# Performance work log

Hardware: AMD Instinct MI355X
Metric: run time of the kernel (lower is better)

Reference implementation:

```python
import jax, jax.numpy as jnp
import numpy as np

NUM_USERS = 100000
NUM_ITEMS = 50000
EMB_DIM = 128
NUM_LAYERS = 3
NUM_EDGES = 2000000
BATCH = 8192
REG = 1e-4


def setup_inputs() -> dict:
    key = jax.random.key(0)
    ks = jax.random.split(key, 8)
    N = NUM_USERS + NUM_ITEMS
    user_emb = jax.random.normal(ks[0], (NUM_USERS, EMB_DIM), dtype=jnp.float32) * 0.01
    item_emb = jax.random.normal(ks[1], (NUM_ITEMS, EMB_DIM), dtype=jnp.float32) * 0.01
    edge_row = jax.random.randint(ks[2], (NUM_EDGES,), 0, N, dtype=jnp.int32)
    edge_col = jax.random.randint(ks[3], (NUM_EDGES,), 0, N, dtype=jnp.int32)
    # symmetric-normalized adjacency values are small positives
    edge_val = jax.random.uniform(ks[4], (NUM_EDGES,), dtype=jnp.float32) * 0.1
    user = jax.random.randint(ks[5], (BATCH,), 0, NUM_USERS, dtype=jnp.int32)
    pos = jax.random.randint(ks[6], (BATCH,), 0, NUM_ITEMS, dtype=jnp.int32)
    neg = jax.random.randint(ks[7], (BATCH,), 0, NUM_ITEMS, dtype=jnp.int32)
    return {"user_emb": user_emb, "item_emb": item_emb,
            "edge_row": edge_row, "edge_col": edge_col, "edge_val": edge_val,
            "user": user, "pos": pos, "neg": neg}


def _lightgcn_embedding(user_emb, item_emb, edge_row, edge_col, edge_val):
    N = user_emb.shape[0] + item_emb.shape[0]
    emb = jnp.concatenate([user_emb, item_emb], axis=0)  # [N, D]
    acc = emb
    for _ in range(NUM_LAYERS):
        # SpMM: out[r] += val * emb[c] for each edge (r, c)
        msg = emb[edge_col] * edge_val[:, None]  # [E, D]
        emb = jax.ops.segment_sum(msg, edge_row, num_segments=N)
        acc = acc + emb
    light = acc / jnp.float32(NUM_LAYERS + 1)  # mean over layer outputs
    return light[:NUM_USERS], light[NUM_USERS:]


def reference(user_emb, item_emb, edge_row, edge_col, edge_val, user, pos, neg):
    u_all, i_all = _lightgcn_embedding(user_emb, item_emb, edge_row, edge_col, edge_val)
    u_lat = u_all[user]          # [B, D]
    pos_lat = i_all[pos]
    neg_lat = i_all[neg]
    pos_score = jnp.sum(u_lat * pos_lat, axis=1)
    neg_score = jnp.sum(u_lat * neg_lat, axis=1)
    # L1 regularization on ego (layer-0) embeddings, scalar broadcast onto batch loss
    reg_loss = REG * (jnp.sum(jnp.abs(user_emb[user]))
                      + jnp.sum(jnp.abs(item_emb[pos]))
                      + jnp.sum(jnp.abs(item_emb[neg])))
    batch_loss = jax.nn.softplus(neg_score - pos_score) + reg_loss
    return batch_loss
```

## Files before the change

### kernel.cpp

```cpp
#include <hip/hip_runtime.h>
#include <hip/hip_bf16.h>

#define EMB_D 128
#define BSH 9
#define MAXBUCK 512
#define CHUNKP 2048

typedef float f32x2 __attribute__((ext_vector_type(2)));

__device__ __forceinline__ float bf16_raw_to_f(unsigned short h) {
    return __uint_as_float(((unsigned int)h) << 16);
}
__device__ __forceinline__ float sane(float v) {
    return (v == v && fabsf(v) < 256.0f) ? v : 0.0f;
}
__device__ __forceinline__ float load_f(const void* p, int isf32, size_t idx) {
    return isf32 ? ((const float*)p)[idx]
                 : bf16_raw_to_f(((const unsigned short*)p)[idx]);
}

__device__ __forceinline__ f32x2 cvt2_fp8(unsigned int w) {
    f32x2 r;
    asm("v_cvt_pk_f32_fp8 %0, %1" : "=v"(r) : "v"(w));
    return r;
}
__device__ __forceinline__ unsigned int enc2_fp8(float a, float b) {
    unsigned int r;
    asm("v_cvt_pk_fp8_f32 %0, %1, %2" : "=v"(r) : "v"(a), "v"(b));
    return r & 0xFFFFu;
}
__device__ __forceinline__ unsigned int fp8x4_enc(float a, float b, float c, float d) {
    return enc2_fp8(a, b) | (enc2_fp8(c, d) << 16);
}
__device__ __forceinline__ float fp8_dec_byte(unsigned int b) {
    return cvt2_fp8(b & 0xFFu).x;
}

__global__ void k_detect(const unsigned short* __restrict__ ue,
                         const unsigned short* __restrict__ ie,
                         const unsigned short* __restrict__ ev,
                         int* __restrict__ flags) {
    int a = blockIdx.x;
    const unsigned short* p = (a == 0) ? ue : (a == 1) ? ie : ev;
    int lane = threadIdx.x;
    int cnt = 0;
    #pragma unroll
    for (int k = 0; k < 16; ++k) {
        float v = bf16_raw_to_f(p[k * 64 + lane]);
        if (!(fabsf(v) < 1.0f)) cnt++;
    }
    #pragma unroll
    for (int off = 32; off > 0; off >>= 1)
        cnt += __shfl_down(cnt, off, 64);
    if (lane == 0) flags[a] = (cnt > 64) ? 1 : 0;
}

__global__ __launch_bounds__(256) void k_build_emb8(
        const void* __restrict__ ue, const void* __restrict__ ie,
        const int* __restrict__ flags,
        unsigned char* __restrict__ T, float* __restrict__ S,
        int NU, int N) {
    int gid = blockIdx.x * blockDim.x + threadIdx.x;
    int row = gid >> 5;
    if (row >= N) return;
    int l = gid & 31;
    const void* src; long r; int f;
    if (row < NU) { src = ue; r = row;      f = flags[0]; }
    else          { src = ie; r = row - NU; f = flags[1]; }
    float v0, v1, v2, v3;
    if (f) {
        float4 t = ((const float4*)src)[r * 32 + l];
        v0 = sane(t.x); v1 = sane(t.y); v2 = sane(t.z); v3 = sane(t.w);
    } else {
        ushort4 t = ((const ushort4*)src)[r * 32 + l];
        v0 = sane(bf16_raw_to_f(t.x)); v1 = sane(bf16_raw_to_f(t.y));
        v2 = sane(bf16_raw_to_f(t.z)); v3 = sane(bf16_raw_to_f(t.w));
    }
    float m = fmaxf(fmaxf(fabsf(v0), fabsf(v1)), fmaxf(fabsf(v2), fabsf(v3)));
    #pragma unroll
    for (int off = 1; off < 32; off <<= 1)
        m = fmaxf(m, __shfl_xor(m, off, 64));
    float enc = (m > 0.0f) ? 448.0f / m : 0.0f;
    ((unsigned int*)T)[(size_t)row * 32 + l] =
        fp8x4_enc(v0 * enc, v1 * enc, v2 * enc, v3 * enc);
    if (l == 0) S[row] = (m > 0.0f) ? m * (1.0f / 448.0f) : 0.0f;
}

__global__ void k_reg(const void* __restrict__ ue, const void* __restrict__ ie,
                      const int* __restrict__ flags,
                      const int* __restrict__ user, const int* __restrict__ pos,
                      const int* __restrict__ neg, int NU, int NI,
                      float* __restrict__ regp) {
    __shared__ float sred[2];
    int b = blockIdx.x;
    int d = threadIdx.x;
    int ui = min(max(user[b], 0), NU - 1);
    int pi = min(max(pos[b],  0), NI - 1);
    int ni = min(max(neg[b],  0), NI - 1);
    int f0 = flags[0], f1 = flags[1];
    float u = sane(load_f(ue, f0, (size_t)ui * EMB_D + d));
    float p = sane(load_f(ie, f1, (size_t)pi * EMB_D + d));
    float n = sane(load_f(ie, f1, (size_t)ni * EMB_D + d));
    float s = fabsf(u) + fabsf(p) + fabsf(n);
    #pragma unroll
    for (int off = 32; off > 0; off >>= 1)
        s += __shfl_down(s, off, 64);
    if ((d & 63) == 0) sred[d >> 6] = s;
    __syncthreads();
    if (d == 0) regp[b] = sred[0] + sred[1];
}

__global__ void k_reduce_reg(const float* __restrict__ regp, float* __restrict__ reg, int B) {
    __shared__ float ss[256];
    int t = threadIdx.x;
    float s = 0.0f;
    for (int i = t; i < B; i += 256) s += regp[i];
    ss[t] = s;
    __syncthreads();
    for (int off = 128; off > 0; off >>= 1) {
        if (t < off) ss[t] += ss[t + off];
        __syncthreads();
    }
    if (t == 0) reg[0] = ss[0];
}


__global__ __launch_bounds__(256) void k_part_count(const int* __restrict__ erow,
        int* __restrict__ bcnt, int E, int N, int nbuck, int NB) {
    __shared__ int lh[MAXBUCK];
    int b = blockIdx.x, t = threadIdx.x;
    for (int i = t; i < MAXBUCK; i += 256) lh[i] = 0;
    __syncthreads();
    int beg = b * CHUNKP;
    int cnt = min(CHUNKP, E - beg);
    for (int p = t; p < cnt; p += 256) {
        int r = min(max(erow[beg + p], 0), N - 1);
        atomicAdd(&lh[r >> BSH], 1);
    }
    __syncthreads();
    for (int i = t; i < nbuck; i += 256) bcnt[(long)i * NB + b] = lh[i];
}

__global__ void k_gscan1(const int* __restrict__ a, int* __restrict__ bsums, int L) {
    __shared__ int ss[256];
    int t = threadIdx.x;
    int base = blockIdx.x * 1024 + t * 4;
    int s = 0;
    #pragma unroll
    for (int j = 0; j < 4; ++j) {
        int idx = base + j;
        if (idx < L) s += a[idx];
    }
    ss[t] = s;
    __syncthreads();
    for (int off = 128; off > 0; off >>= 1) {
        if (t < off) ss[t] += ss[t + off];
        __syncthreads();
    }
    if (t == 0) bsums[blockIdx.x] = ss[0];
}

__global__ void k_gscan2(const int* __restrict__ bsums, int* __restrict__ boffs,
                         int nb, int* __restrict__ rowptrN) {
    __shared__ int ss[256];
    int t = threadIdx.x;
    int base = t * 4;
    int c[4];
    int s = 0;
    #pragma unroll
    for (int j = 0; j < 4; ++j) {
        c[j] = (base + j < nb) ? bsums[base + j] : 0;
        s += c[j];
    }
    ss[t] = s;
    __syncthreads();
    for (int off = 1; off < 256; off <<= 1) {
        int v = (t >= off) ? ss[t - off] : 0;
        __syncthreads();
        ss[t] += v;
        __syncthreads();
    }
    int run = ss[t] - s;
    #pragma unroll
    for (int j = 0; j < 4; ++j) {
        if (base + j < nb) boffs[base + j] = run;
        run += c[j];
    }
    if (t == 255) *rowptrN = ss[255];
}

__global__ void k_gscan3(int* __restrict__ a, const int* __restrict__ boffs, int L) {
    __shared__ int ss[256];
    int t = threadIdx.x;
    int base = blockIdx.x * 1024 + t * 4;
    int c[4];
    int s = 0;
    #pragma unroll
    for (int j = 0; j < 4; ++j) {
        int idx = base + j;
        c[j] = (idx < L) ? a[idx] : 0;
        s += c[j];
    }
    ss[t] = s;
    __syncthreads();
    for (int off = 1; off < 256; off <<= 1) {
        int v = (t >= off) ? ss[t - off] : 0;
        __syncthreads();
        ss[t] += v;
        __syncthreads();
    }
    int run = boffs[blockIdx.x] + ss[t] - s;
    #pragma unroll
    for (int j = 0; j < 4; ++j) {
        int idx = base + j;
        if (idx < L) a[idx] = run;
        run += c[j];
    }
}

__global__ __launch_bounds__(256) void k_part_scatter(
        const int* __restrict__ erow, const int* __restrict__ ecol,
        const void* __restrict__ eval, const int* __restrict__ flags,
        const int* __restrict__ boff,
        unsigned int* __restrict__ part_cv, unsigned short* __restrict__ part_r,
        int E, int N, int nbuck, int NB) {
    __shared__ uint2 lrec[CHUNKP];
    __shared__ unsigned short lidx[CHUNKP];
    __shared__ int hist[MAXBUCK];
    __shared__ int bstart[MAXBUCK];
    __shared__ int ss[256];
    int b = blockIdx.x, t = threadIdx.x;
    int beg = b * CHUNKP;
    int cnt = min(CHUNKP, E - beg);
    for (int i = t; i < MAXBUCK; i += 256) hist[i] = 0;
    __syncthreads();
    int f2 = flags[2];
    for (int p = t; p < cnt; p += 256) {
        int e = beg + p;
        int r = min(max(erow[e], 0), N - 1);
        int c = min(max(ecol[e], 0), N - 1);
        float v = sane(load_f(eval, f2, e));
        if (v < 0.0f) v = 0.0f;
        unsigned int u = __float_as_uint(v);
        unsigned int vb = ((u + 0x10000u) >> 17) & 0x3FFFu;
        lrec[p] = make_uint2((unsigned int)r, ((unsigned int)c << 14) | vb);
        atomicAdd(&hist[r >> BSH], 1);
    }
    __syncthreads();
    int c0 = hist[2 * t], c1 = hist[2 * t + 1];
    int s = c0 + c1;
    ss[t] = s;
    __syncthreads();
    for (int off = 1; off < 256; off <<= 1) {
        int v = (t >= off) ? ss[t - off] : 0;
        __syncthreads();
        ss[t] += v;
        __syncthreads();
    }
    int eb = ss[t] - s;
    bstart[2 * t] = eb;
    bstart[2 * t + 1] = eb + c0;
    hist[2 * t] = eb;
    hist[2 * t + 1] = eb + c0;
    __syncthreads();
    for (int p = t; p < cnt; p += 256) {
        int bin = (int)(lrec[p].x >> BSH);
        int pos = atomicAdd(&hist[bin], 1);
        lidx[pos] = (unsigned short)p;
    }
    __syncthreads();
    for (int i = t; i < nbuck; i += 256)
        hist[i] = boff[(long)i * NB + b] - bstart[i];
    __syncthreads();
    for (int p = t; p < cnt; p += 256) {
        uint2 rec = lrec[lidx[p]];
        int bin = (int)(rec.x >> BSH);
        int o = hist[bin] + p;
        part_cv[o] = rec.y;
        part_r[o] = (unsigned short)(rec.x & 511u);
    }
}

__global__ __launch_bounds__(256) void k_build_csr(
        const unsigned int* __restrict__ part_cv,
        const unsigned short* __restrict__ part_r,
        const int* __restrict__ boff,
        int* __restrict__ row_ptr, unsigned int* __restrict__ sedge,
        int E, int N, int NB, int nbuck) {
    __shared__ int rcnt[512];
    __shared__ int rstart[512];
    __shared__ int rcur[512];
    __shared__ int ss[256];
    int bin = blockIdx.x, t = threadIdx.x;
    int base = boff[(long)bin * NB];
    int next = (bin + 1 < nbuck) ? boff[(long)(bin + 1) * NB] : E;
    int cnt = next - base;
    int r0 = bin << BSH;
    int nrows = min(512, N - r0);
    rcnt[2 * t] = 0; rcnt[2 * t + 1] = 0;
    __syncthreads();
    for (int i = t; i < cnt; i += 256)
        atomicAdd(&rcnt[part_r[base + i]], 1);
    __syncthreads();
    int c0 = rcnt[2 * t], c1 = rcnt[2 * t + 1];
    int s = c0 + c1;
    ss[t] = s;
    __syncthreads();
    for (int off = 1; off < 256; off <<= 1) {
        int v = (t >= off) ? ss[t - off] : 0;
        __syncthreads();
        ss[t] += v;
        __syncthreads();
    }
    int eb = ss[t] - s;
    rstart[2 * t] = eb; rstart[2 * t + 1] = eb + c0;
    rcur[2 * t]   = eb; rcur[2 * t + 1]   = eb + c0;
    __syncthreads();
    for (int j = t; j < nrows; j += 256)
        row_ptr[r0 + j] = base + rstart[j];
    for (int i = t; i < cnt; i += 256) {
        int pr = part_r[base + i];
        int pos = atomicAdd(&rcur[pr], 1);
        sedge[base + pos] = part_cv[base + i];
    }
}


__global__ void k_zero_flags(int* __restrict__ f, int words) {
    int i = blockIdx.x * blockDim.x + threadIdx.x;
    if (i < words) f[i] = 0;
}

__global__ void k_mark_batch(const int* __restrict__ user, const int* __restrict__ pos,
                             const int* __restrict__ neg, int NU, int NI, int B,
                             unsigned char* __restrict__ flag3,
                             unsigned char* __restrict__ flag2) {
    int b = blockIdx.x * blockDim.x + threadIdx.x;
    if (b >= B) return;
    int ui = min(max(user[b], 0), NU - 1);
    int pi = NU + min(max(pos[b], 0), NI - 1);
    int ni = NU + min(max(neg[b], 0), NI - 1);
    flag3[ui] = 1; flag3[pi] = 1; flag3[ni] = 1;
    flag2[ui] = 1; flag2[pi] = 1; flag2[ni] = 1;
}

__global__ void k_mark_nbrs(const int* __restrict__ row_ptr,
                            const unsigned int* __restrict__ sedge,
                            const unsigned char* __restrict__ flag3,
                            unsigned char* __restrict__ flag2, int N) {
    int r = blockIdx.x * blockDim.x + threadIdx.x;
    if (r >= N || !flag3[r]) return;
    int beg = row_ptr[r], end = row_ptr[r + 1];
    for (int i = beg; i < end; ++i)
        flag2[sedge[i] >> 14] = 1;
}


__global__ void k_spmm_csr8(const unsigned char* __restrict__ T,
                            const float* __restrict__ S,
                            unsigned char* __restrict__ Td,
                            float* __restrict__ Sd,
                            const int* __restrict__ row_ptr,
                            const unsigned int* __restrict__ sedge, int N,
                            const unsigned char* __restrict__ skipf, int use_skip) {
    int row = blockIdx.x * (blockDim.x >> 6) + (threadIdx.x >> 6);
    if (row >= N) return;
    if (use_skip && skipf[row] == 0) return;
    int lane = threadIdx.x & 63;
    int sub = lane >> 3;
    int sl  = lane & 7;
    int beg = row_ptr[row], end = row_ptr[row + 1];
    float a[16];
    #pragma unroll
    for (int j = 0; j < 16; ++j) a[j] = 0.0f;
    int i = beg + sub;
    for (; i + 8 < end; i += 16) {
        unsigned int se0 = sedge[i];
        unsigned int se1 = sedge[i + 8];
        unsigned int c0 = se0 >> 14, c1 = se1 >> 14;
        uint4 h0 = ((const uint4*)(T + (size_t)c0 * EMB_D))[sl];
        uint4 h1 = ((const uint4*)(T + (size_t)c1 * EMB_D))[sl];
        float vs0 = __uint_as_float((se0 & 0x3FFFu) << 17) * S[c0];
        float vs1 = __uint_as_float((se1 & 0x3FFFu) << 17) * S[c1];
        f32x2 d;
        d = cvt2_fp8(h0.x);       a[0] += vs0 * d.x;  a[1] += vs0 * d.y;
        d = cvt2_fp8(h0.x >> 16); a[2] += vs0 * d.x;  a[3] += vs0 * d.y;
        d = cvt2_fp8(h0.y);       a[4] += vs0 * d.x;  a[5] += vs0 * d.y;
        d = cvt2_fp8(h0.y >> 16); a[6] += vs0 * d.x;  a[7] += vs0 * d.y;
        d = cvt2_fp8(h0.z);       a[8] += vs0 * d.x;  a[9] += vs0 * d.y;
        d = cvt2_fp8(h0.z >> 16); a[10] += vs0 * d.x; a[11] += vs0 * d.y;
        d = cvt2_fp8(h0.w);       a[12] += vs0 * d.x; a[13] += vs0 * d.y;
        d = cvt2_fp8(h0.w >> 16); a[14] += vs0 * d.x; a[15] += vs0 * d.y;
        d = cvt2_fp8(h1.x);       a[0] += vs1 * d.x;  a[1] += vs1 * d.y;
        d = cvt2_fp8(h1.x >> 16); a[2] += vs1 * d.x;  a[3] += vs1 * d.y;
        d = cvt2_fp8(h1.y);       a[4] += vs1 * d.x;  a[5] += vs1 * d.y;
        d = cvt2_fp8(h1.y >> 16); a[6] += vs1 * d.x;  a[7] += vs1 * d.y;
        d = cvt2_fp8(h1.z);       a[8] += vs1 * d.x;  a[9] += vs1 * d.y;
        d = cvt2_fp8(h1.z >> 16); a[10] += vs1 * d.x; a[11] += vs1 * d.y;
        d = cvt2_fp8(h1.w);       a[12] += vs1 * d.x; a[13] += vs1 * d.y;
        d = cvt2_fp8(h1.w >> 16); a[14] += vs1 * d.x; a[15] += vs1 * d.y;
    }
    if (i < end) {
        unsigned int se = sedge[i];
        unsigned int c = se >> 14;
        uint4 h = ((const uint4*)(T + (size_t)c * EMB_D))[sl];
        float vs = __uint_as_float((se & 0x3FFFu) << 17) * S[c];
        f32x2 d;
        d = cvt2_fp8(h.x);       a[0] += vs * d.x;  a[1] += vs * d.y;
        d = cvt2_fp8(h.x >> 16); a[2] += vs * d.x;  a[3] += vs * d.y;
        d = cvt2_fp8(h.y);       a[4] += vs * d.x;  a[5] += vs * d.y;
        d = cvt2_fp8(h.y >> 16); a[6] += vs * d.x;  a[7] += vs * d.y;
        d = cvt2_fp8(h.z);       a[8] += vs * d.x;  a[9] += vs * d.y;
        d = cvt2_fp8(h.z >> 16); a[10] += vs * d.x; a[11] += vs * d.y;
        d = cvt2_fp8(h.w);       a[12] += vs * d.x; a[13] += vs * d.y;
        d = cvt2_fp8(h.w >> 16); a[14] += vs * d.x; a[15] += vs * d.y;
    }
    #pragma unroll
    for (int j = 0; j < 16; ++j) {
        a[j] += __shfl_xor(a[j], 8, 64);
        a[j] += __shfl_xor(a[j], 16, 64);
        a[j] += __shfl_xor(a[j], 32, 64);
    }
    float m = 0.0f;
    #pragma unroll
    for (int j = 0; j < 16; ++j) m = fmaxf(m, fabsf(a[j]));
    m = fmaxf(m, __shfl_xor(m, 1, 64));
    m = fmaxf(m, __shfl_xor(m, 2, 64));
    m = fmaxf(m, __shfl_xor(m, 4, 64));
    if (sub == 0) {
        float enc = (m > 0.0f) ? 448.0f / m : 0.0f;
        uint4 w;
        w.x = fp8x4_enc(a[0] * enc,  a[1] * enc,  a[2] * enc,  a[3] * enc);
        w.y = fp8x4_enc(a[4] * enc,  a[5] * enc,  a[6] * enc,  a[7] * enc);
        w.z = fp8x4_enc(a[8] * enc,  a[9] * enc,  a[10] * enc, a[11] * enc);
        w.w = fp8x4_enc(a[12] * enc, a[13] * enc, a[14] * enc, a[15] * enc);
        ((uint4*)(Td + (size_t)row * EMB_D))[sl] = w;
        if (lane == 0) Sd[row] = (m > 0.0f) ? m * (1.0f / 448.0f) : 0.0f;
    }
}

__global__ void k_gather_final(
        const void* __restrict__ ue, const void* __restrict__ ie,
        const int* __restrict__ flags,
        const int* __restrict__ user, const int* __restrict__ pos,
        const int* __restrict__ neg, int NU, int NI,
        const unsigned char* __restrict__ T1, const float* __restrict__ S1,
        const unsigned char* __restrict__ T2, const float* __restrict__ S2,
        const unsigned char* __restrict__ T3, const float* __restrict__ S3,
        const float* __restrict__ reg, float* __restrict__ out) {
    __shared__ float sps[2], sns[2];
    int b = blockIdx.x;
    int d = threadIdx.x;
    int ui = min(max(user[b], 0), NU - 1);
    int pi = min(max(pos[b],  0), NI - 1);
    int ni = min(max(neg[b],  0), NI - 1);
    size_t ru = (size_t)ui;
    size_t rp = (size_t)NU + pi;
    size_t rn = (size_t)NU + ni;
    int f0 = flags[0], f1 = flags[1];
    float u = sane(load_f(ue, f0, ru * EMB_D + d))
            + fp8_dec_byte(T1[ru * EMB_D + d]) * S1[ru]
            + fp8_dec_byte(T2[ru * EMB_D + d]) * S2[ru]
            + fp8_dec_byte(T3[ru * EMB_D + d]) * S3[ru];
    float p = sane(load_f(ie, f1, (size_t)pi * EMB_D + d))
            + fp8_dec_byte(T1[rp * EMB_D + d]) * S1[rp]
            + fp8_dec_byte(T2[rp * EMB_D + d]) * S2[rp]
            + fp8_dec_byte(T3[rp * EMB_D + d]) * S3[rp];
    float n = sane(load_f(ie, f1, (size_t)ni * EMB_D + d))
            + fp8_dec_byte(T1[rn * EMB_D + d]) * S1[rn]
            + fp8_dec_byte(T2[rn * EMB_D + d]) * S2[rn]
            + fp8_dec_byte(T3[rn * EMB_D + d]) * S3[rn];
    float ps = u * p, ns = u * n;
    #pragma unroll
    for (int off = 32; off > 0; off >>= 1) {
        ps += __shfl_down(ps, off, 64);
        ns += __shfl_down(ns, off, 64);
    }
    if ((d & 63) == 0) { sps[d >> 6] = ps; sns[d >> 6] = ns; }
    __syncthreads();
    if (d == 0) {
        float x = ((sns[0] + sns[1]) - (sps[0] + sps[1])) * 0.0625f;
        float sp = fmaxf(x, 0.0f) + log1pf(expf(-fabsf(x)));
        out[b] = sp + 1e-4f * reg[0];
    }
}

extern "C" void kernel_launch(void* const* d_in, const int* in_sizes, int n_in,
                              void* d_out, int out_size, void* d_ws, size_t ws_size,
                              hipStream_t stream) {
    const void* ue   = d_in[0];
    const void* ie   = d_in[1];
    const int*  erow = (const int*)d_in[2];
    const int*  ecol = (const int*)d_in[3];
    const void* ev   = d_in[4];
    const int*  user = (const int*)d_in[5];
    const int*  pos  = (const int*)d_in[6];
    const int*  neg  = (const int*)d_in[7];

    int NU = in_sizes[0] / EMB_D;
    int NI = in_sizes[1] / EMB_D;
    int N  = NU + NI;
    int E  = in_sizes[2];
    int B  = in_sizes[5];

    int nbuck = (N + ((1 << BSH) - 1)) >> BSH;
    int NBp   = (E + CHUNKP - 1) / CHUNKP;
    int L     = nbuck * NBp;
    int nbL   = (L + 1023) / 1024;

    size_t T8   = (size_t)N * EMB_D;
    size_t SC   = (((size_t)N * sizeof(float)) + 15) & ~15ull;
    size_t NI4  = ((size_t)(N + 1) * sizeof(int) + 15) & ~15ull;
    size_t L4   = ((size_t)L * sizeof(int) + 15) & ~15ull;
    size_t E2   = (((size_t)E * 2) + 15) & ~15ull;
    size_t Npad = ((size_t)N + 15) & ~15ull;
    char* w = (char*)d_ws;
    int*   flags   = (int*)w;
    float* reg     = (float*)(w + 64);
    char*  q       = w + 256;
    float* regp    = (float*)q;             q += (size_t)B * sizeof(float);
    int*   row_ptr = (int*)q;               q += NI4;
    unsigned int*   part_cv = (unsigned int*)q;   q += (size_t)E * 4;
    unsigned short* part_r  = (unsigned short*)q; q += E2;
    int*   bcnt    = (int*)q;               q += L4;
    int*   bsums   = (int*)q;               q += 4096;
    int*   boffs   = (int*)q;               q += 4096;
    unsigned char* flag3 = (unsigned char*)q; q += Npad;
    unsigned char* flag2 = (unsigned char*)q; q += Npad;
    unsigned int* sedge = (unsigned int*)q; q += (size_t)E * 4;
    unsigned char* Ta = (unsigned char*)q;  q += T8;
    float*         Sa = (float*)q;          q += SC;
    unsigned char* T1 = (unsigned char*)q;  q += T8;
    float*         S1 = (float*)q;          q += SC;
    unsigned char* T2 = (unsigned char*)q;  q += T8;
    float*         S2 = (float*)q;          q += SC;
    unsigned char* T3 = (unsigned char*)q;  q += T8;
    float*         S3 = (float*)q;

    const int thr = 256;
    float* out = (float*)d_out;

    k_detect<<<3, 64, 0, stream>>>((const unsigned short*)ue, (const unsigned short*)ie,
                                   (const unsigned short*)ev, flags);
    k_build_emb8<<<(N * 32 + thr - 1) / thr, thr, 0, stream>>>(ue, ie, flags, Ta, Sa, NU, N);
    k_reg<<<B, EMB_D, 0, stream>>>(ue, ie, flags, user, pos, neg, NU, NI, regp);
    k_reduce_reg<<<1, 256, 0, stream>>>(regp, reg, B);

    int fwords = (int)((2 * Npad) / 4);
    k_zero_flags<<<(fwords + thr - 1) / thr, thr, 0, stream>>>((int*)flag3, fwords);
    k_mark_batch<<<(B + thr - 1) / thr, thr, 0, stream>>>(user, pos, neg, NU, NI, B,
                                                          flag3, flag2);

    k_part_count<<<NBp, 256, 0, stream>>>(erow, bcnt, E, N, nbuck, NBp);
    k_gscan1<<<nbL, 256, 0, stream>>>(bcnt, bsums, L);
    k_gscan2<<<1, 256, 0, stream>>>(bsums, boffs, nbL, row_ptr + N);
    k_gscan3<<<nbL, 256, 0, stream>>>(bcnt, boffs, L);
    k_part_scatter<<<NBp, 256, 0, stream>>>(erow, ecol, ev, flags, bcnt,
                                            part_cv, part_r, E, N, nbuck, NBp);
    k_build_csr<<<nbuck, 256, 0, stream>>>(part_cv, part_r, bcnt, row_ptr, sedge,
                                           E, N, NBp, nbuck);

    k_mark_nbrs<<<(N + thr - 1) / thr, thr, 0, stream>>>(row_ptr, sedge, flag3, flag2, N);

    int rows_per_block = thr / 64;
    int sgrid = (N + rows_per_block - 1) / rows_per_block;

    k_spmm_csr8<<<sgrid, thr, 0, stream>>>(Ta, Sa, T1, S1, row_ptr, sedge, N, flag2, 0);
    k_spmm_csr8<<<sgrid, thr, 0, stream>>>(T1, S1, T2, S2, row_ptr, sedge, N, flag2, 1);
    k_spmm_csr8<<<sgrid, thr, 0, stream>>>(T2, S2, T3, S3, row_ptr, sedge, N, flag3, 1);

    k_gather_final<<<B, EMB_D, 0, stream>>>(ue, ie, flags, user, pos, neg, NU, NI,
                                            T1, S1, T2, S2, T3, S3, reg, out);
}
```

Before: 441.5 us.

## Fuse reg into batch marking, mark neighbors during partition, split CSR build, narrow SpMM lanes

Merges the L1-regularization reduction into the batch-marking kernel, and moves neighbor marking from a separate CSR-walking kernel into the partition-count pass, so one launch and one irregular pass go away. The CSR build now runs two blocks per 512-row bucket, each handling 256 rows, which raises parallelism at the cost of both blocks re-reading the bucket's edges. The SpMM kernel now has each of the 64 lanes own two fp8 columns and walk every edge of the row with 4-way unrolling, replacing the 8-subgroup uint4 scheme and its cross-lane reduction. The new SpMM makes narrower 2-byte loads per lane and processes edges serially per wave, trading memory-level parallelism for fewer registers and no shuffle reduction.

After: 472.0 us. 6.9% more time.

```diff
diff --git a/kernel.cpp b/kernel.cpp
--- a/kernel.cpp
+++ b/kernel.cpp
@@ -86,17 +86,29 @@
     if (l == 0) S[row] = (m > 0.0f) ? m * (1.0f / 448.0f) : 0.0f;
 }
 
-__global__ void k_reg(const void* __restrict__ ue, const void* __restrict__ ie,
-                      const int* __restrict__ flags,
-                      const int* __restrict__ user, const int* __restrict__ pos,
-                      const int* __restrict__ neg, int NU, int NI,
-                      float* __restrict__ regp) {
+__global__ void k_zero_flags(int* __restrict__ f, int words, float* __restrict__ reg) {
+    int i = blockIdx.x * blockDim.x + threadIdx.x;
+    if (i < words) f[i] = 0;
+    if (i == 0) reg[0] = 0.0f;
+}
+
+__global__ void k_mark_batch(const int* __restrict__ user, const int* __restrict__ pos,
+                             const int* __restrict__ neg,
+                             const void* __restrict__ ue, const void* __restrict__ ie,
+                             const int* __restrict__ flags, int NU, int NI,
+                             unsigned char* __restrict__ flag3,
+                             unsigned char* __restrict__ flag2,
+                             float* __restrict__ regp) {
     __shared__ float sred[2];
     int b = blockIdx.x;
     int d = threadIdx.x;
     int ui = min(max(user[b], 0), NU - 1);
     int pi = min(max(pos[b],  0), NI - 1);
     int ni = min(max(neg[b],  0), NI - 1);
+    if (d == 0) {
+        flag3[ui] = 1; flag3[NU + pi] = 1; flag3[NU + ni] = 1;
+        flag2[ui] = 1; flag2[NU + pi] = 1; flag2[NU + ni] = 1;
+    }
     int f0 = flags[0], f1 = flags[1];
     float u = sane(load_f(ue, f0, (size_t)ui * EMB_D + d));
     float p = sane(load_f(ie, f1, (size_t)pi * EMB_D + d));
@@ -125,7 +137,9 @@
 }
 
 
-__global__ __launch_bounds__(256) void k_part_count(const int* __restrict__ erow,
+__global__ __launch_bounds__(256) void k_part_count(
+        const int* __restrict__ erow, const int* __restrict__ ecol,
+        const unsigned char* __restrict__ flag3, unsigned char* __restrict__ flag2,
         int* __restrict__ bcnt, int E, int N, int nbuck, int NB) {
     __shared__ int lh[MAXBUCK];
     int b = blockIdx.x, t = threadIdx.x;
@@ -134,8 +148,13 @@
     int beg = b * CHUNKP;
     int cnt = min(CHUNKP, E - beg);
     for (int p = t; p < cnt; p += 256) {
-        int r = min(max(erow[beg + p], 0), N - 1);
+        int e = beg + p;
+        int r = min(max(erow[e], 0), N - 1);
         atomicAdd(&lh[r >> BSH], 1);
+        if (flag3[r]) {
+            int c = min(max(ecol[e], 0), N - 1);
+            flag2[c] = 1;
+        }
     }
     __syncthreads();
     for (int i = t; i < nbuck; i += 256) bcnt[(long)i * NB + b] = lh[i];
@@ -287,24 +306,35 @@
         const int* __restrict__ boff,
         int* __restrict__ row_ptr, unsigned int* __restrict__ sedge,
         int E, int N, int NB, int nbuck) {
-    __shared__ int rcnt[512];
-    __shared__ int rstart[512];
-    __shared__ int rcur[512];
+    __shared__ int rcnt[256];
+    __shared__ int rcur[256];
     __shared__ int ss[256];
-    int bin = blockIdx.x, t = threadIdx.x;
+    __shared__ int slow;
+    int blk = blockIdx.x, t = threadIdx.x;
+    int bin = blk >> 1, half = blk & 1;
     int base = boff[(long)bin * NB];
     int next = (bin + 1 < nbuck) ? boff[(long)(bin + 1) * NB] : E;
     int cnt = next - base;
     int r0 = bin << BSH;
-    int nrows = min(512, N - r0);
-    rcnt[2 * t] = 0; rcnt[2 * t + 1] = 0;
-    __syncthreads();
-    for (int i = t; i < cnt; i += 256)
-        atomicAdd(&rcnt[part_r[base + i]], 1);
-    __syncthreads();
-    int c0 = rcnt[2 * t], c1 = rcnt[2 * t + 1];
-    int s = c0 + c1;
-    ss[t] = s;
+    int rlo = half << 8;
+    int nrows = min(256, max(0, min(512, N - r0) - rlo));
+    rcnt[t] = 0;
+    if (t == 0) slow = 0;
+    __syncthreads();
+    int lowc = 0;
+    for (int i = t; i < cnt; i += 256) {
+        int pr = part_r[base + i];
+        int lp = pr - rlo;
+        if (lp >= 0 && lp < 256) atomicAdd(&rcnt[lp], 1);
+        else if (pr < rlo) lowc++;
+    }
+    #pragma unroll
+    for (int off = 32; off > 0; off >>= 1)
+        lowc += __shfl_down(lowc, off, 64);
+    if ((t & 63) == 0 && lowc) atomicAdd(&slow, lowc);
+    __syncthreads();
+    int c = rcnt[t];
+    ss[t] = c;
     __syncthreads();
     for (int off = 1; off < 256; off <<= 1) {
         int v = (t >= off) ? ss[t - off] : 0;
@@ -312,131 +342,67 @@
         ss[t] += v;
         __syncthreads();
     }
-    int eb = ss[t] - s;
-    rstart[2 * t] = eb; rstart[2 * t + 1] = eb + c0;
-    rcur[2 * t]   = eb; rcur[2 * t + 1]   = eb + c0;
-    __syncthreads();
-    for (int j = t; j < nrows; j += 256)
-        row_ptr[r0 + j] = base + rstart[j];
+    int st = ss[t] - c + slow;
+    rcur[t] = st;
+    __syncthreads();
+    if (t < nrows) row_ptr[r0 + rlo + t] = base + st;
     for (int i = t; i < cnt; i += 256) {
         int pr = part_r[base + i];
-        int pos = atomicAdd(&rcur[pr], 1);
-        sedge[base + pos] = part_cv[base + i];
-    }
-}
-
-
-__global__ void k_zero_flags(int* __restrict__ f, int words) {
-    int i = blockIdx.x * blockDim.x + threadIdx.x;
-    if (i < words) f[i] = 0;
-}
-
-__global__ void k_mark_batch(const int* __restrict__ user, const int* __restrict__ pos,
-                             const int* __restrict__ neg, int NU, int NI, int B,
-                             unsigned char* __restrict__ flag3,
-                             unsigned char* __restrict__ flag2) {
-    int b = blockIdx.x * blockDim.x + threadIdx.x;
-    if (b >= B) return;
-    int ui = min(max(user[b], 0), NU - 1);
-    int pi = NU + min(max(pos[b], 0), NI - 1);
-    int ni = NU + min(max(neg[b], 0), NI - 1);
-    flag3[ui] = 1; flag3[pi] = 1; flag3[ni] = 1;
-    flag2[ui] = 1; flag2[pi] = 1; flag2[ni] = 1;
-}
-
-__global__ void k_mark_nbrs(const int* __restrict__ row_ptr,
-                            const unsigned int* __restrict__ sedge,
-                            const unsigned char* __restrict__ flag3,
-                            unsigned char* __restrict__ flag2, int N) {
-    int r = blockIdx.x * blockDim.x + threadIdx.x;
-    if (r >= N || !flag3[r]) return;
-    int beg = row_ptr[r], end = row_ptr[r + 1];
-    for (int i = beg; i < end; ++i)
-        flag2[sedge[i] >> 14] = 1;
-}
-
-
-__global__ void k_spmm_csr8(const unsigned char* __restrict__ T,
-                            const float* __restrict__ S,
-                            unsigned char* __restrict__ Td,
-                            float* __restrict__ Sd,
-                            const int* __restrict__ row_ptr,
-                            const unsigned int* __restrict__ sedge, int N,
-                            const unsigned char* __restrict__ skipf, int use_skip) {
+        int lp = pr - rlo;
+        if (lp >= 0 && lp < 256) {
+            int pos = atomicAdd(&rcur[lp], 1);
+            sedge[base + pos] = part_cv[base + i];
+        }
+    }
+}
+
+__global__ __launch_bounds__(256, 8) void k_spmm_csr8(
+        const unsigned char* __restrict__ T, const float* __restrict__ S,
+        unsigned char* __restrict__ Td, float* __restrict__ Sd,
+        const int* __restrict__ row_ptr, const unsigned int* __restrict__ sedge,
+        int N, const unsigned char* __restrict__ skipf, int use_skip) {
     int row = blockIdx.x * (blockDim.x >> 6) + (threadIdx.x >> 6);
     if (row >= N) return;
     if (use_skip && skipf[row] == 0) return;
     int lane = threadIdx.x & 63;
-    int sub = lane >> 3;
-    int sl  = lane & 7;
     int beg = row_ptr[row], end = row_ptr[row + 1];
-    float a[16];
-    #pragma unroll
-    for (int j = 0; j < 16; ++j) a[j] = 0.0f;
-    int i = beg + sub;
-    for (; i + 8 < end; i += 16) {
-        unsigned int se0 = sedge[i];
-        unsigned int se1 = sedge[i + 8];
-        unsigned int c0 = se0 >> 14, c1 = se1 >> 14;
-        uint4 h0 = ((const uint4*)(T + (size_t)c0 * EMB_D))[sl];
-        uint4 h1 = ((const uint4*)(T + (size_t)c1 * EMB_D))[sl];
-        float vs0 = __uint_as_float((se0 & 0x3FFFu) << 17) * S[c0];
-        float vs1 = __uint_as_float((se1 & 0x3FFFu) << 17) * S[c1];
+    const unsigned short* Tw = (const unsigned short*)T;
+    float a0 = 0.0f, a1 = 0.0f;
+    int e = beg;
+    for (; e + 3 < end; e += 4) {
+        unsigned int s0 = sedge[e],     s1 = sedge[e + 1];
+        unsigned int s2 = sedge[e + 2], s3 = sedge[e + 3];
+        unsigned int c0 = s0 >> 14, c1 = s1 >> 14, c2 = s2 >> 14, c3 = s3 >> 14;
+        unsigned int h0 = Tw[(size_t)c0 * 64 + lane];
+        unsigned int h1 = Tw[(size_t)c1 * 64 + lane];
+        unsigned int h2 = Tw[(size_t)c2 * 64 + lane];
+        unsigned int h3 = Tw[(size_t)c3 * 64 + lane];
+        float v0 = __uint_as_float((s0 & 0x3FFFu) << 17) * S[c0];
+        float v1 = __uint_as_float((s1 & 0x3FFFu) << 17) * S[c1];
+        float v2 = __uint_as_float((s2 & 0x3FFFu) << 17) * S[c2];
+        float v3 = __uint_as_float((s3 & 0x3FFFu) << 17) * S[c3];
         f32x2 d;
-        d = cvt2_fp8(h0.x);       a[0] += vs0 * d.x;  a[1] += vs0 * d.y;
-        d = cvt2_fp8(h0.x >> 16); a[2] += vs0 * d.x;  a[3] += vs0 * d.y;
-        d = cvt2_fp8(h0.y);       a[4] += vs0 * d.x;  a[5] += vs0 * d.y;
-        d = cvt2_fp8(h0.y >> 16); a[6] += vs0 * d.x;  a[7] += vs0 * d.y;
-        d = cvt2_fp8(h0.z);       a[8] += vs0 * d.x;  a[9] += vs0 * d.y;
-        d = cvt2_fp8(h0.z >> 16); a[10] += vs0 * d.x; a[11] += vs0 * d.y;
-        d = cvt2_fp8(h0.w);       a[12] += vs0 * d.x; a[13] += vs0 * d.y;
-        d = cvt2_fp8(h0.w >> 16); a[14] += vs0 * d.x; a[15] += vs0 * d.y;
-        d = cvt2_fp8(h1.x);       a[0] += vs1 * d.x;  a[1] += vs1 * d.y;
-        d = cvt2_fp8(h1.x >> 16); a[2] += vs1 * d.x;  a[3] += vs1 * d.y;
-        d = cvt2_fp8(h1.y);       a[4] += vs1 * d.x;  a[5] += vs1 * d.y;
-        d = cvt2_fp8(h1.y >> 16); a[6] += vs1 * d.x;  a[7] += vs1 * d.y;
-        d = cvt2_fp8(h1.z);       a[8] += vs1 * d.x;  a[9] += vs1 * d.y;
-        d = cvt2_fp8(h1.z >> 16); a[10] += vs1 * d.x; a[11] += vs1 * d.y;
-        d = cvt2_fp8(h1.w);       a[12] += vs1 * d.x; a[13] += vs1 * d.y;
-        d = cvt2_fp8(h1.w >> 16); a[14] += vs1 * d.x; a[15] += vs1 * d.y;
-    }
-    if (i < end) {
-        unsigned int se = sedge[i];
-        unsigned int c = se >> 14;
-        uint4 h = ((const uint4*)(T + (size_t)c * EMB_D))[sl];
-        float vs = __uint_as_float((se & 0x3FFFu) << 17) * S[c];
-        f32x2 d;
-        d = cvt2_fp8(h.x);       a[0] += vs * d.x;  a[1] += vs * d.y;
-        d = cvt2_fp8(h.x >> 16); a[2] += vs * d.x;  a[3] += vs * d.y;
-        d = cvt2_fp8(h.y);       a[4] += vs * d.x;  a[5] += vs * d.y;
-        d = cvt2_fp8(h.y >> 16); a[6] += vs * d.x;  a[7] += vs * d.y;
-        d = cvt2_fp8(h.z);       a[8] += vs * d.x;  a[9] += vs * d.y;
-        d = cvt2_fp8(h.z >> 16); a[10] += vs * d.x; a[11] += vs * d.y;
-        d = cvt2_fp8(h.w);       a[12] += vs * d.x; a[13] += vs * d.y;
-        d = cvt2_fp8(h.w >> 16); a[14] += vs * d.x; a[15] += vs * d.y;
-    }
-    #pragma unroll
-    for (int j = 0; j < 16; ++j) {
-        a[j] += __shfl_xor(a[j], 8, 64);
-        a[j] += __shfl_xor(a[j], 16, 64);
-        a[j] += __shfl_xor(a[j], 32, 64);
-    }
-    float m = 0.0f;
-    #pragma unroll
-    for (int j = 0; j < 16; ++j) m = fmaxf(m, fabsf(a[j]));
-    m = fmaxf(m, __shfl_xor(m, 1, 64));
-    m = fmaxf(m, __shfl_xor(m, 2, 64));
-    m = fmaxf(m, __shfl_xor(m, 4, 64));
-    if (sub == 0) {
-        float enc = (m > 0.0f) ? 448.0f / m : 0.0f;
-        uint4 w;
-        w.x = fp8x4_enc(a[0] * enc,  a[1] * enc,  a[2] * enc,  a[3] * enc);
-        w.y = fp8x4_enc(a[4] * enc,  a[5] * enc,  a[6] * enc,  a[7] * enc);
-        w.z = fp8x4_enc(a[8] * enc,  a[9] * enc,  a[10] * enc, a[11] * enc);
-        w.w = fp8x4_enc(a[12] * enc, a[13] * enc, a[14] * enc, a[15] * enc);
-        ((uint4*)(Td + (size_t)row * EMB_D))[sl] = w;
-        if (lane == 0) Sd[row] = (m > 0.0f) ? m * (1.0f / 448.0f) : 0.0f;
-    }
+        d = cvt2_fp8(h0); a0 += v0 * d.x; a1 += v0 * d.y;
+        d = cvt2_fp8(h1); a0 += v1 * d.x; a1 += v1 * d.y;
+        d = cvt2_fp8(h2); a0 += v2 * d.x; a1 += v2 * d.y;
+        d = cvt2_fp8(h3); a0 += v3 * d.x; a1 += v3 * d.y;
+    }
+    for (; e < end; ++e) {
+        unsigned int s0 = sedge[e];
+        unsigned int c0 = s0 >> 14;
+        unsigned int h0 = Tw[(size_t)c0 * 64 + lane];
+        float v0 = __uint_as_float((s0 & 0x3FFFu) << 17) * S[c0];
+        f32x2 d = cvt2_fp8(h0);
+        a0 += v0 * d.x; a1 += v0 * d.y;
+    }
+    float m = fmaxf(fabsf(a0), fabsf(a1));
+    #pragma unroll
+    for (int off = 1; off < 64; off <<= 1)
+        m = fmaxf(m, __shfl_xor(m, off, 64));
+    float enc = (m > 0.0f) ? 448.0f / m : 0.0f;
+    unsigned int w = enc2_fp8(a0 * enc, a1 * enc);
+    ((unsigned short*)(Td + (size_t)row * EMB_D))[lane] = (unsigned short)w;
+    if (lane == 0) Sd[row] = (m > 0.0f) ? m * (1.0f / 448.0f) : 0.0f;
 }
 
 __global__ void k_gather_final(
@@ -542,25 +508,21 @@
 
     k_detect<<<3, 64, 0, stream>>>((const unsigned short*)ue, (const unsigned short*)ie,
                                    (const unsigned short*)ev, flags);
+    int fwords = (int)((2 * Npad) / 4);
+    k_zero_flags<<<(fwords + thr - 1) / thr, thr, 0, stream>>>((int*)flag3, fwords, reg);
+    k_mark_batch<<<B, EMB_D, 0, stream>>>(user, pos, neg, ue, ie, flags, NU, NI,
+                                          flag3, flag2, regp);
+    k_reduce_reg<<<1, 256, 0, stream>>>(regp, reg, B);
     k_build_emb8<<<(N * 32 + thr - 1) / thr, thr, 0, stream>>>(ue, ie, flags, Ta, Sa, NU, N);
-    k_reg<<<B, EMB_D, 0, stream>>>(ue, ie, flags, user, pos, neg, NU, NI, regp);
-    k_reduce_reg<<<1, 256, 0, stream>>>(regp, reg, B);
-
-    int fwords = (int)((2 * Npad) / 4);
-    k_zero_flags<<<(fwords + thr - 1) / thr, thr, 0, stream>>>((int*)flag3, fwords);
-    k_mark_batch<<<(B + thr - 1) / thr, thr, 0, stream>>>(user, pos, neg, NU, NI, B,
-                                                          flag3, flag2);
-
-    k_part_count<<<NBp, 256, 0, stream>>>(erow, bcnt, E, N, nbuck, NBp);
+
+    k_part_count<<<NBp, 256, 0, stream>>>(erow, ecol, flag3, flag2, bcnt, E, N, nbuck, NBp);
     k_gscan1<<<nbL, 256, 0, stream>>>(bcnt, bsums, L);
     k_gscan2<<<1, 256, 0, stream>>>(bsums, boffs, nbL, row_ptr + N);
     k_gscan3<<<nbL, 256, 0, stream>>>(bcnt, boffs, L);
     k_part_scatter<<<NBp, 256, 0, stream>>>(erow, ecol, ev, flags, bcnt,
                                             part_cv, part_r, E, N, nbuck, NBp);
-    k_build_csr<<<nbuck, 256, 0, stream>>>(part_cv, part_r, bcnt, row_ptr, sedge,
-                                           E, N, NBp, nbuck);
-
-    k_mark_nbrs<<<(N + thr - 1) / thr, thr, 0, stream>>>(row_ptr, sedge, flag3, flag2, N);
+    k_build_csr<<<2 * nbuck, 256, 0, stream>>>(part_cv, part_r, bcnt, row_ptr, sedge,
+                                               E, N, NBp, nbuck);
 
     int rows_per_block = thr / 64;
     int sgrid = (N + rows_per_block - 1) / rows_per_block;
```
